# Kernel optimization log

Hardware: AMD Instinct MI355X
Metric: run time of the kernel (lower is better)

Reference implementation:

```python
import jax, jax.numpy as jnp
import numpy as np

B, T, F, U = 256, 2048, 64, 64
KEEP = 0.5  # recurrent_dropout=0.5 -> keep prob 0.5


def setup_inputs() -> dict:
    key = jax.random.key(0)
    ks = jax.random.split(key, 7)
    inputs = jax.random.normal(ks[0], (B, T, F), dtype=jnp.float32)
    kernel = jax.random.normal(ks[1], (F, 3 * U), dtype=jnp.float32) * 0.1
    recurrent_kernel = jax.random.normal(ks[2], (U, 3 * U), dtype=jnp.float32) * 0.1
    bias = jax.random.normal(ks[3], (2, 3 * U), dtype=jnp.float32) * 0.1
    dense_w = jax.random.normal(ks[4], (U, 1), dtype=jnp.float32) * 0.1
    dense_b = jnp.zeros((1,), dtype=jnp.float32)
    # Keras recurrent dropout: one fixed mask per gate (z, r, h), constant over time,
    # applied to h_prev before the recurrent matmul; inverted-dropout scaling.
    bern = jax.random.bernoulli(ks[5], KEEP, (3, B, U)).astype(jnp.float32)
    rec_mask = bern / KEEP
    return {
        "inputs": inputs,
        "kernel": kernel,
        "recurrent_kernel": recurrent_kernel,
        "bias": bias,
        "dense_w": dense_w,
        "dense_b": dense_b,
        "rec_mask": rec_mask,
    }


def _gru_dense(inputs, kernel, recurrent_kernel, bias, dense_w, dense_b, rec_mask):
    # Precompute input projections for all timesteps: [B, T, 3U]
    x_proj = jnp.einsum("btf,fg->btg", inputs, kernel) + bias[0]
    Uz, Ur, Uh = jnp.split(recurrent_kernel, 3, axis=1)  # each [U, U]
    bz, br, bh = jnp.split(bias[1], 3)                   # each [U]
    mz, mr, mh = rec_mask[0], rec_mask[1], rec_mask[2]   # each [B, U]

    def step(h, xt):
        xz, xr, xh = jnp.split(xt, 3, axis=-1)  # each [B, U]
        z = jax.nn.sigmoid(xz + (h * mz) @ Uz + bz)
        r = jax.nn.sigmoid(xr + (h * mr) @ Ur + br)
        hh = jnp.tanh(xh + r * ((h * mh) @ Uh + bh))  # reset_after=True
        h_new = z * h + (1.0 - z) * hh
        return h_new, None

    h0 = jnp.zeros((B, U), dtype=inputs.dtype)
    h_last, _ = jax.lax.scan(step, h0, jnp.swapaxes(x_proj, 0, 1))  # scan over T
    return h_last @ dense_w + dense_b  # [B, 1]


def reference(inputs, kernel, recurrent_kernel, bias, dense_w, dense_b, rec_mask):
    return _gru_dense(inputs, kernel, recurrent_kernel, bias, dense_w, dense_b, rec_mask)
```

## Files before the change

kernel.cpp:

```cpp
#include <hip/hip_runtime.h>

#define BB 256
#define TT 2048
#define FF 64
#define UU 64
#define C3 192
#define CH 16

__device__ __forceinline__ float readlane_f(float v, int lane) {
    return __int_as_float(__builtin_amdgcn_readlane(__float_as_int(v), lane));
}
__device__ __forceinline__ float fast_sigmoid(float x) {
    return __builtin_amdgcn_rcpf(1.0f + __expf(-x));
}
__device__ __forceinline__ float fast_tanh(float x) {
    return 1.0f - 2.0f * __builtin_amdgcn_rcpf(__expf(2.0f * x) + 1.0f);
}
__device__ __forceinline__ float shflx(float v, int m) { return __shfl_xor(v, m, 64); }

#define REP16(M) M(0) M(1) M(2) M(3) M(4) M(5) M(6) M(7) \
                 M(8) M(9) M(10) M(11) M(12) M(13) M(14) M(15)
#define XREP8(M, I) M(I,0) M(I,1) M(I,2) M(I,3) M(I,4) M(I,5) M(I,6) M(I,7)
#define XREP64(M) XREP8(M,0) XREP8(M,1) XREP8(M,2) XREP8(M,3) \
                  XREP8(M,4) XREP8(M,5) XREP8(M,6) XREP8(M,7)

__global__ __launch_bounds__(256)
void xproj(const float* __restrict__ in, const float* __restrict__ kmat,
           const float* __restrict__ bias, float* __restrict__ xp,
           int t0, int tc) {
    const int lane = threadIdx.x & 63;
    const int wave = (int)((blockIdx.x * blockDim.x + threadIdx.x) >> 6);
    const int nwaves = (int)((gridDim.x * blockDim.x) >> 6);

#define DECLK(I,J) float kz_##I##J, kr_##I##J, kh_##I##J;
    XREP64(DECLK)
#define INITK(I,J) { const int f_ = (I)*8+(J); \
    kz_##I##J = kmat[f_ * C3 + lane]; \
    kr_##I##J = kmat[f_ * C3 + 64 + lane]; \
    kh_##I##J = kmat[f_ * C3 + 128 + lane]; }
    XREP64(INITK)

    const float bz  = bias[lane]       + bias[C3 + lane];
    const float br  = bias[64 + lane]  + bias[C3 + 64 + lane];
    const float bh0 = bias[128 + lane];

    const int rows = BB * tc;
    for (int r = wave; r < rows; r += nwaves) {
        const int bq = r / tc;
        const int t  = t0 + (r - bq * tc);
        const float a = in[((size_t)bq * TT + t) * FF + lane];
        float az = bz, ar = br, ah = bh0;
#define STEPK(I,J) { const float s_ = readlane_f(a, (I)*8+(J)); \
        az = fmaf(s_, kz_##I##J, az); ar = fmaf(s_, kr_##I##J, ar); \
        ah = fmaf(s_, kh_##I##J, ah); }
        XREP64(STEPK)
        float* o = xp + (size_t)r * C3;
        o[lane] = az; o[64 + lane] = ar; o[128 + lane] = ah;
    }
}

__global__ void __launch_bounds__(256, 1)
gru_scan(const float* __restrict__ xp, const float* __restrict__ rk,
         const float* __restrict__ bias, const float* __restrict__ mask,
         const float* __restrict__ dw, const float* __restrict__ db,
         float* __restrict__ hws, float* __restrict__ out,
         int tc, int first, int last) {
    __shared__ __align__(16) float hb[2][64];
    __shared__ __align__(16) float ring[2][CH][C3];

    const int b    = blockIdx.x;
    const int tid  = threadIdx.x;
    const int lane = tid & 63;
    const int wv   = tid >> 6;
    const int sub  = lane >> 4;
    const int u    = lane & 15;
    const int j    = (wv << 4) + u;
    const int i0   = sub << 4;

    const float* mzp = mask;
    const float* mrp = mask + (size_t)BB * UU;
    const float* mhp = mask + (size_t)2 * BB * UU;
#define DECLUW(K) float uz##K, ur##K, uh##K;
    REP16(DECLUW)
#define INITUW(K) { const int i_ = i0 + (K); \
    uz##K = rk[i_ * C3 + j]       * mzp[(size_t)b * UU + i_]; \
    ur##K = rk[i_ * C3 + 64 + j]  * mrp[(size_t)b * UU + i_]; \
    uh##K = rk[i_ * C3 + 128 + j] * mhp[(size_t)b * UU + i_]; }
    REP16(INITUW)

    const float bh1j = bias[C3 + 128 + j];

    const float* __restrict__ xpb = xp + (size_t)b * tc * C3;

    {
        const float4* src = (const float4*)xpb;
        const float4 v0 = src[tid], v1 = src[tid + 256], v2 = src[tid + 512];
        float4* dst = (float4*)&ring[0][0][0];
        dst[tid] = v0; dst[tid + 256] = v1; dst[tid + 512] = v2;
    }
    float hown = first ? 0.0f : hws[(size_t)b * UU + j];
    if (wv == 0) hb[0][lane] = first ? 0.0f : hws[(size_t)b * UU + lane];
    __syncthreads();

#pragma unroll 1
    for (int e = 0; e < tc; ++e) {
        const int  c  = e >> 4;
        const bool st = ((e & 15) == 0) && ((c + 1) * CH < tc);

        float4 g0, g1, g2;
        if (st) {
            const float4* src = (const float4*)(xpb + (size_t)(c + 1) * CH * C3);
            g0 = src[tid]; g1 = src[tid + 256]; g2 = src[tid + 512];
        }

        const float4 hA = *(const float4*)&hb[e & 1][i0];
        const float4 hB = *(const float4*)&hb[e & 1][i0 + 4];
        const float4 hC = *(const float4*)&hb[e & 1][i0 + 8];
        const float4 hD = *(const float4*)&hb[e & 1][i0 + 12];

        const float* xrow = &ring[c & 1][e & 15][0];
        const float xz = xrow[j], xr = xrow[64 + j], xh = xrow[128 + j];

        float hz = 0.f, hr = 0.f, hah = 0.f;
#define FMA_H(K, HV) { hz = fmaf(HV, uz##K, hz); hr = fmaf(HV, ur##K, hr); \
                       hah = fmaf(HV, uh##K, hah); }
        FMA_H(0,  hA.x) FMA_H(1,  hA.y) FMA_H(2,  hA.z) FMA_H(3,  hA.w)
        FMA_H(4,  hB.x) FMA_H(5,  hB.y) FMA_H(6,  hB.z) FMA_H(7,  hB.w)
        FMA_H(8,  hC.x) FMA_H(9,  hC.y) FMA_H(10, hC.z) FMA_H(11, hC.w)
        FMA_H(12, hD.x) FMA_H(13, hD.y) FMA_H(14, hD.z) FMA_H(15, hD.w)

        float sz = hz, sr = hr, sah = hah;
        { const float t0 = shflx(sz, 16), t1 = shflx(sr, 16), t2 = shflx(sah, 16);
          sz += t0; sr += t1; sah += t2; }
        { const float t0 = shflx(sz, 32), t1 = shflx(sr, 32), t2 = shflx(sah, 32);
          sz += t0; sr += t1; sah += t2; }

        const float z  = fast_sigmoid(sz + xz);
        const float r  = fast_sigmoid(sr + xr);
        const float hh = fast_tanh(fmaf(r, sah + bh1j, xh));
        hown = fmaf(z, hown - hh, hh);

        if (sub == 0) hb[(e + 1) & 1][j] = hown;

        if (st) {
            float4* dst = (float4*)&ring[(c + 1) & 1][0][0];
            dst[tid] = g0; dst[tid + 256] = g1; dst[tid + 512] = g2;
        }
        __syncthreads();
    }

    if (last) {
        if (wv == 0) {
            float p = hb[tc & 1][lane] * dw[lane];
#pragma unroll
            for (int o = 32; o > 0; o >>= 1) p += __shfl_down(p, o, 64);
            if (lane == 0) out[b] = p + db[0];
        }
    } else {
        if (wv == 0) hws[(size_t)b * UU + lane] = hb[tc & 1][lane];
    }
}

__global__ void __launch_bounds__(256, 1)
gru_fused7(const float* __restrict__ in, const float* __restrict__ kmat,
           const float* __restrict__ rk, const float* __restrict__ bias,
           const float* __restrict__ mask, const float* __restrict__ dw,
           const float* __restrict__ db, float* __restrict__ out) {
    __shared__ __align__(16) float hb[2][64];
    __shared__ __align__(16) float ab[2][32][FF];

    const int b    = blockIdx.x;
    const int lane = threadIdx.x & 63;
    const int wv   = threadIdx.x >> 6;
    const int sub  = lane >> 4;
    const int u    = lane & 15;
    const int j    = (wv << 4) + u;
    const int i0   = sub << 4;

    const float* mzp = mask;
    const float* mrp = mask + (size_t)BB * UU;
    const float* mhp = mask + (size_t)2 * BB * UU;
#define DECLW7(K) float fuz##K, fur##K, fuh##K, fkz##K, fkr##K, fkh##K;
    REP16(DECLW7)
#define INITW7(K) { const int i_ = i0 + (K); \
    fuz##K = rk[i_ * C3 + j]       * mzp[(size_t)b * UU + i_]; \
    fur##K = rk[i_ * C3 + 64 + j]  * mrp[(size_t)b * UU + i_]; \
    fuh##K = rk[i_ * C3 + 128 + j] * mhp[(size_t)b * UU + i_]; \
    fkz##K = kmat[i_ * C3 + j]; \
    fkr##K = kmat[i_ * C3 + 64 + j]; \
    fkh##K = kmat[i_ * C3 + 128 + j]; }
    REP16(INITW7)

    const float bzj  = bias[j]       + bias[C3 + j];
    const float brj  = bias[64 + j]  + bias[C3 + 64 + j];
    const float bh0j = bias[128 + j];
    const float bh1j = bias[C3 + 128 + j];

    const float* __restrict__ inb = in + (size_t)b * TT * FF;
    {
        const float* src = inb + (size_t)(wv * 8) * FF + lane;
        const float t0 = src[0 * FF], t1 = src[1 * FF], t2 = src[2 * FF],
                    t3 = src[3 * FF], t4 = src[4 * FF], t5 = src[5 * FF],
                    t6 = src[6 * FF], t7 = src[7 * FF];
        float* dst = &ab[0][wv * 8][lane];
        dst[0 * FF] = t0; dst[1 * FF] = t1; dst[2 * FF] = t2; dst[3 * FF] = t3;
        dst[4 * FF] = t4; dst[5 * FF] = t5; dst[6 * FF] = t6; dst[7 * FF] = t7;
    }
    if (wv == 0) hb[0][lane] = 0.0f;
    __syncthreads();

    float4 aA = *(const float4*)&ab[0][0][i0];
    float4 aB = *(const float4*)&ab[0][0][i0 + 4];
    float4 aC = *(const float4*)&ab[0][0][i0 + 8];
    float4 aD = *(const float4*)&ab[0][0][i0 + 12];
    float hown = 0.0f;

#pragma unroll 1
    for (int e = 0; e < TT; ++e) {
        const int  c  = e >> 5;
        const bool st = ((e & 31) == 0) && (c + 1 < TT / 32);
        float g0, g1, g2, g3, g4, g5, g6, g7;
        if (st) {
            const float* src = inb + ((size_t)(c + 1) * 32 + wv * 8) * FF + lane;
            g0 = src[0 * FF]; g1 = src[1 * FF]; g2 = src[2 * FF]; g3 = src[3 * FF];
            g4 = src[4 * FF]; g5 = src[5 * FF]; g6 = src[6 * FF]; g7 = src[7 * FF];
        }
        const float4 hA = *(const float4*)&hb[e & 1][i0];
        const float4 hB = *(const float4*)&hb[e & 1][i0 + 4];
        const float4 hC = *(const float4*)&hb[e & 1][i0 + 8];
        const float4 hD = *(const float4*)&hb[e & 1][i0 + 12];

        float az = 0.f, ar = 0.f, axh = 0.f;
#define FMA_A7(K, AV) { az = fmaf(AV, fkz##K, az); ar = fmaf(AV, fkr##K, ar); \
                        axh = fmaf(AV, fkh##K, axh); }
        FMA_A7(0,  aA.x) FMA_A7(1,  aA.y) FMA_A7(2,  aA.z) FMA_A7(3,  aA.w)
        FMA_A7(4,  aB.x) FMA_A7(5,  aB.y) FMA_A7(6,  aB.z) FMA_A7(7,  aB.w)
        FMA_A7(8,  aC.x) FMA_A7(9,  aC.y) FMA_A7(10, aC.z) FMA_A7(11, aC.w)
        FMA_A7(12, aD.x) FMA_A7(13, aD.y) FMA_A7(14, aD.z) FMA_A7(15, aD.w)

        float hz = 0.f, hr = 0.f, hah = 0.f;
#define FMA_H7(K, HV) { hz = fmaf(HV, fuz##K, hz); hr = fmaf(HV, fur##K, hr); \
                        hah = fmaf(HV, fuh##K, hah); }
        FMA_H7(0,  hA.x) FMA_H7(1,  hA.y) FMA_H7(2,  hA.z) FMA_H7(3,  hA.w)
        FMA_H7(4,  hB.x) FMA_H7(5,  hB.y) FMA_H7(6,  hB.z) FMA_H7(7,  hB.w)
        FMA_H7(8,  hC.x) FMA_H7(9,  hC.y) FMA_H7(10, hC.z) FMA_H7(11, hC.w)
        FMA_H7(12, hD.x) FMA_H7(13, hD.y) FMA_H7(14, hD.z) FMA_H7(15, hD.w)

        float sz = az + hz, sr = ar + hr, sxh = axh, sah = hah;
        { const float t0 = shflx(sz, 16), t1 = shflx(sr, 16),
                      t2 = shflx(sxh, 16), t3 = shflx(sah, 16);
          sz += t0; sr += t1; sxh += t2; sah += t3; }
        { const float t0 = shflx(sz, 32), t1 = shflx(sr, 32),
                      t2 = shflx(sxh, 32), t3 = shflx(sah, 32);
          sz += t0; sr += t1; sxh += t2; sah += t3; }

        const float z  = fast_sigmoid(sz + bzj);
        const float r  = fast_sigmoid(sr + brj);
        const float hh = fast_tanh(fmaf(r, sah + bh1j, sxh + bh0j));
        hown = fmaf(z, hown - hh, hh);
        if (sub == 0) hb[(e + 1) & 1][j] = hown;

        const int rn = (e + 1 < TT) ? (e + 1) : (TT - 1);
        const float* ap = &ab[(rn >> 5) & 1][rn & 31][i0];
        aA = *(const float4*)(ap);
        aB = *(const float4*)(ap + 4);
        aC = *(const float4*)(ap + 8);
        aD = *(const float4*)(ap + 12);

        if (st) {
            float* dst = &ab[(c + 1) & 1][wv * 8][lane];
            dst[0 * FF] = g0; dst[1 * FF] = g1; dst[2 * FF] = g2; dst[3 * FF] = g3;
            dst[4 * FF] = g4; dst[5 * FF] = g5; dst[6 * FF] = g6; dst[7 * FF] = g7;
        }
        __syncthreads();
    }

    if (wv == 0) {
        float p = hb[0][lane] * dw[lane];
#pragma unroll
        for (int o = 32; o > 0; o >>= 1) p += __shfl_down(p, o, 64);
        if (lane == 0) out[b] = p + db[0];
    }
}

extern "C" void kernel_launch(void* const* d_in, const int* in_sizes, int n_in,
                              void* d_out, int out_size, void* d_ws, size_t ws_size,
                              hipStream_t stream) {
    (void)in_sizes; (void)n_in; (void)out_size;
    const float* inputs = (const float*)d_in[0];
    const float* kmat   = (const float*)d_in[1];
    const float* rk     = (const float*)d_in[2];
    const float* bias   = (const float*)d_in[3];
    const float* dw     = (const float*)d_in[4];
    const float* db     = (const float*)d_in[5];
    const float* mask   = (const float*)d_in[6];
    float* out = (float*)d_out;

    const size_t h_bytes   = (size_t)BB * UU * sizeof(float);
    const size_t row_bytes = (size_t)BB * C3 * sizeof(float);

    int cap = 0;
    if (ws_size > h_bytes)
        cap = (int)((ws_size - h_bytes) / row_bytes) & ~(CH - 1);
    if (cap > TT) cap = TT;

    if (cap >= 256) {
        float* hws = (float*)d_ws;
        float* xp  = (float*)((char*)d_ws + h_bytes);
        const int nch  = (TT + cap - 1) / cap;
        int base = (TT + nch - 1) / nch;
        base = (base + CH - 1) & ~(CH - 1);
        int t0 = 0;
        while (t0 < TT) {
            const int cur = (TT - t0) < base ? (TT - t0) : base;
            xproj<<<512, 256, 0, stream>>>(inputs, kmat, bias, xp, t0, cur);
            gru_scan<<<BB, 256, 0, stream>>>(xp, rk, bias, mask, dw, db, hws, out,
                                             cur, t0 == 0 ? 1 : 0,
                                             (t0 + cur == TT) ? 1 : 0);
            t0 += cur;
        }
    } else {
        gru_fused7<<<BB, 256, 0, stream>>>(inputs, kmat, rk, bias, mask, dw, db, out);
    }
}
```

Measured before the change: 1.159 ms.

## Run GRU scan as a single wave per batch with readlane broadcast

Replaces the 4-wave recurrent scan, which used LDS h exchange, cross-lane shuffles and a block barrier every step, with a single 64-lane wave per batch row. Each lane holds the full 64x3 column of the masked recurrent weights in registers (192 VGPRs) and broadcasts h via readlane, so no barrier or LDS traffic is needed. It also prefetches x projections four steps ahead into registers and doubles the xproj grid. The cost is 64 serial FMA triples per step per lane instead of 16, plus heavy register pressure, with only 256 waves occupying the GPU.

```diff
diff --git a/kernel.cpp b/kernel.cpp
--- a/kernel.cpp
+++ b/kernel.cpp
@@ -5,7 +5,7 @@
 #define FF 64
 #define UU 64
 #define C3 192
-#define CH 16
+#define CHX 16
 
 __device__ __forceinline__ float readlane_f(float v, int lane) {
     return __int_as_float(__builtin_amdgcn_readlane(__float_as_int(v), lane));
@@ -59,105 +59,70 @@
     }
 }
 
-__global__ void __launch_bounds__(256, 1)
-gru_scan(const float* __restrict__ xp, const float* __restrict__ rk,
-         const float* __restrict__ bias, const float* __restrict__ mask,
-         const float* __restrict__ dw, const float* __restrict__ db,
-         float* __restrict__ hws, float* __restrict__ out,
-         int tc, int first, int last) {
-    __shared__ __align__(16) float hb[2][64];
-    __shared__ __align__(16) float ring[2][CH][C3];
-
-    const int b    = blockIdx.x;
-    const int tid  = threadIdx.x;
-    const int lane = tid & 63;
-    const int wv   = tid >> 6;
-    const int sub  = lane >> 4;
-    const int u    = lane & 15;
-    const int j    = (wv << 4) + u;
-    const int i0   = sub << 4;
+__global__ void __launch_bounds__(64, 1)
+__attribute__((amdgpu_waves_per_eu(1, 1)))
+gru_scan1(const float* __restrict__ xp, const float* __restrict__ rk,
+          const float* __restrict__ bias, const float* __restrict__ mask,
+          const float* __restrict__ dw, const float* __restrict__ db,
+          float* __restrict__ hws, float* __restrict__ out,
+          int tc, int first, int last) {
+    const int b = blockIdx.x;
+    const int j = threadIdx.x;
 
     const float* mzp = mask;
     const float* mrp = mask + (size_t)BB * UU;
     const float* mhp = mask + (size_t)2 * BB * UU;
-#define DECLUW(K) float uz##K, ur##K, uh##K;
-    REP16(DECLUW)
-#define INITUW(K) { const int i_ = i0 + (K); \
-    uz##K = rk[i_ * C3 + j]       * mzp[(size_t)b * UU + i_]; \
-    ur##K = rk[i_ * C3 + 64 + j]  * mrp[(size_t)b * UU + i_]; \
-    uh##K = rk[i_ * C3 + 128 + j] * mhp[(size_t)b * UU + i_]; }
-    REP16(INITUW)
-
-    const float bh1j = bias[C3 + 128 + j];
+#define DECLU(I,J) float uz_##I##J, ur_##I##J, uh_##I##J;
+    XREP64(DECLU)
+#define INITU(I,J) { const int i_ = (I)*8+(J); \
+    uz_##I##J = rk[i_ * C3 + j]       * mzp[(size_t)b * UU + i_]; \
+    ur_##I##J = rk[i_ * C3 + 64 + j]  * mrp[(size_t)b * UU + i_]; \
+    uh_##I##J = rk[i_ * C3 + 128 + j] * mhp[(size_t)b * UU + i_]; }
+    XREP64(INITU)
+
+    const float bh1 = bias[C3 + 128 + j];
 
     const float* __restrict__ xpb = xp + (size_t)b * tc * C3;
 
-    {
-        const float4* src = (const float4*)xpb;
-        const float4 v0 = src[tid], v1 = src[tid + 256], v2 = src[tid + 512];
-        float4* dst = (float4*)&ring[0][0][0];
-        dst[tid] = v0; dst[tid + 256] = v1; dst[tid + 512] = v2;
-    }
-    float hown = first ? 0.0f : hws[(size_t)b * UU + j];
-    if (wv == 0) hb[0][lane] = first ? 0.0f : hws[(size_t)b * UU + lane];
-    __syncthreads();
+    float h = first ? 0.0f : hws[(size_t)b * UU + j];
+
+    float xz0 = xpb[0 * C3 + j], xr0 = xpb[0 * C3 + 64 + j], xh0 = xpb[0 * C3 + 128 + j];
+    float xz1 = xpb[1 * C3 + j], xr1 = xpb[1 * C3 + 64 + j], xh1 = xpb[1 * C3 + 128 + j];
+    float xz2 = xpb[2 * C3 + j], xr2 = xpb[2 * C3 + 64 + j], xh2 = xpb[2 * C3 + 128 + j];
+    float xz3 = xpb[3 * C3 + j], xr3 = xpb[3 * C3 + 64 + j], xh3 = xpb[3 * C3 + 128 + j];
+
+#define SFMA(I,J) { const float hs_ = readlane_f(h, (I)*8+(J)); \
+    az = fmaf(hs_, uz_##I##J, az); ar = fmaf(hs_, ur_##I##J, ar); \
+    ah = fmaf(hs_, uh_##I##J, ah); }
+
+#define SUBSTEP(S) { \
+    float az = 0.0f, ar = 0.0f, ah = 0.0f; \
+    XREP64(SFMA) \
+    const float z  = fast_sigmoid(az + xz##S); \
+    const float r  = fast_sigmoid(ar + xr##S); \
+    const float hh = fast_tanh(fmaf(r, ah + bh1, xh##S)); \
+    h = fmaf(z, h - hh, hh); \
+    const int tn_ = t_ + 4; \
+    if (tn_ < tc) { \
+        const float* p_ = xpb + (size_t)tn_ * C3; \
+        xz##S = p_[j]; xr##S = p_[64 + j]; xh##S = p_[128 + j]; \
+    } }
 
 #pragma unroll 1
-    for (int e = 0; e < tc; ++e) {
-        const int  c  = e >> 4;
-        const bool st = ((e & 15) == 0) && ((c + 1) * CH < tc);
-
-        float4 g0, g1, g2;
-        if (st) {
-            const float4* src = (const float4*)(xpb + (size_t)(c + 1) * CH * C3);
-            g0 = src[tid]; g1 = src[tid + 256]; g2 = src[tid + 512];
-        }
-
-        const float4 hA = *(const float4*)&hb[e & 1][i0];
-        const float4 hB = *(const float4*)&hb[e & 1][i0 + 4];
-        const float4 hC = *(const float4*)&hb[e & 1][i0 + 8];
-        const float4 hD = *(const float4*)&hb[e & 1][i0 + 12];
-
-        const float* xrow = &ring[c & 1][e & 15][0];
-        const float xz = xrow[j], xr = xrow[64 + j], xh = xrow[128 + j];
-
-        float hz = 0.f, hr = 0.f, hah = 0.f;
-#define FMA_H(K, HV) { hz = fmaf(HV, uz##K, hz); hr = fmaf(HV, ur##K, hr); \
-                       hah = fmaf(HV, uh##K, hah); }
-        FMA_H(0,  hA.x) FMA_H(1,  hA.y) FMA_H(2,  hA.z) FMA_H(3,  hA.w)
-        FMA_H(4,  hB.x) FMA_H(5,  hB.y) FMA_H(6,  hB.z) FMA_H(7,  hB.w)
-        FMA_H(8,  hC.x) FMA_H(9,  hC.y) FMA_H(10, hC.z) FMA_H(11, hC.w)
-        FMA_H(12, hD.x) FMA_H(13, hD.y) FMA_H(14, hD.z) FMA_H(15, hD.w)
-
-        float sz = hz, sr = hr, sah = hah;
-        { const float t0 = shflx(sz, 16), t1 = shflx(sr, 16), t2 = shflx(sah, 16);
-          sz += t0; sr += t1; sah += t2; }
-        { const float t0 = shflx(sz, 32), t1 = shflx(sr, 32), t2 = shflx(sah, 32);
-          sz += t0; sr += t1; sah += t2; }
-
-        const float z  = fast_sigmoid(sz + xz);
-        const float r  = fast_sigmoid(sr + xr);
-        const float hh = fast_tanh(fmaf(r, sah + bh1j, xh));
-        hown = fmaf(z, hown - hh, hh);
-
-        if (sub == 0) hb[(e + 1) & 1][j] = hown;
-
-        if (st) {
-            float4* dst = (float4*)&ring[(c + 1) & 1][0][0];
-            dst[tid] = g0; dst[tid + 256] = g1; dst[tid + 512] = g2;
-        }
-        __syncthreads();
+    for (int tb = 0; tb < tc; tb += 4) {
+        { const int t_ = tb + 0; SUBSTEP(0) }
+        { const int t_ = tb + 1; SUBSTEP(1) }
+        { const int t_ = tb + 2; SUBSTEP(2) }
+        { const int t_ = tb + 3; SUBSTEP(3) }
     }
 
     if (last) {
-        if (wv == 0) {
-            float p = hb[tc & 1][lane] * dw[lane];
+        float p = h * dw[j];
 #pragma unroll
-            for (int o = 32; o > 0; o >>= 1) p += __shfl_down(p, o, 64);
-            if (lane == 0) out[b] = p + db[0];
-        }
+        for (int o = 32; o > 0; o >>= 1) p += __shfl_down(p, o, 64);
+        if (j == 0) out[b] = p + db[0];
     } else {
-        if (wv == 0) hws[(size_t)b * UU + lane] = hb[tc & 1][lane];
+        hws[(size_t)b * UU + j] = h;
     }
 }
 
@@ -301,7 +266,7 @@
 
     int cap = 0;
     if (ws_size > h_bytes)
-        cap = (int)((ws_size - h_bytes) / row_bytes) & ~(CH - 1);
+        cap = (int)((ws_size - h_bytes) / row_bytes) & ~(CHX - 1);
     if (cap > TT) cap = TT;
 
     if (cap >= 256) {
@@ -309,12 +274,12 @@
         float* xp  = (float*)((char*)d_ws + h_bytes);
         const int nch  = (TT + cap - 1) / cap;
         int base = (TT + nch - 1) / nch;
-        base = (base + CH - 1) & ~(CH - 1);
+        base = (base + CHX - 1) & ~(CHX - 1);
         int t0 = 0;
         while (t0 < TT) {
             const int cur = (TT - t0) < base ? (TT - t0) : base;
-            xproj<<<512, 256, 0, stream>>>(inputs, kmat, bias, xp, t0, cur);
-            gru_scan<<<BB, 256, 0, stream>>>(xp, rk, bias, mask, dw, db, hws, out,
+            xproj<<<1024, 256, 0, stream>>>(inputs, kmat, bias, xp, t0, cur);
+            gru_scan1<<<BB, 64, 0, stream>>>(xp, rk, bias, mask, dw, db, hws, out,
                                              cur, t0 == 0 ? 1 : 0,
                                              (t0 + cur == TT) ? 1 : 0);
             t0 += cur;
```

Result: slower. 1.434 ms (+23.7%).
